# Kernel optimization log

Measured on AMD Instinct MI355X. Metric: run time of the kernel, lower is better.

The kernel has to match this reference:

```python
import jax, jax.numpy as jnp
import numpy as np

LEN_M = 131328   # (data_dim+1) * d_h = 513 * 256
D_H = 256
N_MC = 64
DATA_DIM_P1 = 513
N = 4096


def setup_inputs() -> dict:
    key = jax.random.key(0)
    k1, k2, k3, k4 = jax.random.split(key, 4)
    params = jax.random.normal(k1, (2 * LEN_M,), dtype=jnp.float32)
    W1 = jax.random.normal(k2, (D_H + 1,), dtype=jnp.float32)
    x = jax.random.normal(k3, (N, DATA_DIM_P1), dtype=jnp.float32)
    eps = jax.random.normal(k4, (N_MC,), dtype=jnp.float32)
    return {"params": params, "W1": W1, "x": x, "eps": eps}


def reference(params, W1, x, eps):
    # split variational params into means and (relu'd) variances
    m_w0 = params[:LEN_M]                                  # [len_m]
    v_w0 = jax.nn.relu(params[LEN_M:]) + 1e-6              # [len_m]
    # reparameterized MC sampling; NOTE: torch code draws ONE scalar eps per
    # MC sample (randn(m_w0[0].shape) is scalar), shared across all weights.
    samps_w0 = m_w0[:, None] + eps[None, :] * jnp.sqrt(v_w0)[:, None]  # [len_m, M]
    W0 = samps_w0.reshape(DATA_DIM_P1, D_H, N_MC)          # [d+1, h, M]
    # fused batched GEMM replacing the d_h * num_MC_samps tiny matmuls
    x_w0 = jnp.einsum('nd,dhm->nhm', x, W0)                # [N, h, M]
    z = jax.nn.relu(x_w0)
    ones = jnp.ones((x.shape[0], 1, N_MC), dtype=x.dtype)
    z = jnp.concatenate([ones, z], axis=1)                 # [N, h+1, M]
    pred_samps = jnp.einsum('nhm,h->nm', z, W1)            # [N, M]
    return pred_samps, m_w0, v_w0
```

## Files before the change

### kernel.cpp

```cpp
#include <hip/hip_runtime.h>
#include <hip/hip_bf16.h>
#include <math.h>

#define LEN_M   131328
#define D_P1    513
#define NROW    4096
#define PRED_ELEMS (NROW * 64)

typedef __attribute__((ext_vector_type(8))) short short8;
typedef __attribute__((ext_vector_type(4))) float floatx4;
typedef __attribute__((ext_vector_type(2))) float v2f;

__device__ __forceinline__ void gl_lds16(const void* g, void* l)
{
    __builtin_amdgcn_global_load_lds(
        (const __attribute__((address_space(1))) unsigned int*)g,
        (__attribute__((address_space(3))) unsigned int*)l, 16, 0, 0);
}

__device__ __forceinline__ unsigned short bf16b(float f)
{
    __hip_bfloat16 h = __float2bfloat16(f);
    return *(unsigned short*)&h;
}

__global__ __launch_bounds__(256) void prep_kernel(
    const float* __restrict__ params, float* __restrict__ out,
    __hip_bfloat16* __restrict__ wcbt)
{
    __shared__ unsigned short T[64][65];
    const int bid = blockIdx.x;
    const int t   = threadIdx.x;

    if (bid < 513) {
        int i = bid * 256 + t;
        float m = params[i];
        float v = fmaxf(params[LEN_M + i], 0.0f) + 1e-6f;
        out[PRED_ELEMS + i]         = m;
        out[PRED_ELEMS + LEN_M + i] = v;
        return;
    }
    if (bid < 769) {
        int i = (bid - 513) * 1024 + t * 4;
        float4 z = {0.f, 0.f, 0.f, 0.f};
        *(float4*)(out + i) = z;
        return;
    }

    const int b2 = bid - 769;
    const int k0 = (b2 & 7) * 64;
    const int c0 = (b2 >> 3) * 64;
    const int hh = t & 63, kb = t >> 6;
    const bool spart = (c0 >= 256);
    const int hbase = c0 & 255;
    const float* src = params + (spart ? LEN_M : 0);

    #pragma unroll 4
    for (int p = 0; p < 16; ++p) {
        int kk = p * 4 + kb;
        float v = src[(k0 + kk) * 256 + hbase + hh];
        if (spart) v = sqrtf(fmaxf(v, 0.0f) + 1e-6f);
        T[kk][hh] = bf16b(v);
    }
    __syncthreads();

    const int cc = t >> 2, kq = t & 3;
    short8 lo, hi;
    #pragma unroll
    for (int j = 0; j < 8; ++j) lo[j] = (short)T[kq * 16 + j][cc];
    #pragma unroll
    for (int j = 0; j < 8; ++j) hi[j] = (short)T[kq * 16 + 8 + j][cc];

    const int cR = c0 + cc;
    const int g1 = (k0 >> 3) + 2 * kq;
    const int g2 = g1 + 1;
    const int d1 = (g1 >> 3) * 4096 + cR * 8 + ((g1 & 7) ^ (cR & 7));
    const int d2 = (g2 >> 3) * 4096 + cR * 8 + ((g2 & 7) ^ (cR & 7));
    short* wb = (short*)wcbt;
    *(short8*)(wb + d1 * 8) = lo;
    *(short8*)(wb + d2 * 8) = hi;
}

__global__ __launch_bounds__(512) void main_kernel(
    const __hip_bfloat16* __restrict__ wcbt, const float* __restrict__ params,
    const float* __restrict__ x, const float* __restrict__ W1,
    const float* __restrict__ eps, float* __restrict__ out)
{
    extern __shared__ char smem[];
    char*  Ap = smem + 32768;
    float* Cl = (float*)smem;

    const int t = threadIdx.x;
    const int w = t >> 6, lane = t & 63;
    const int lane15 = lane & 15, quad = lane >> 4;
    const int ax7 = lane15 & 7;
    const int q  = blockIdx.x & 3;
    const int bm = (blockIdx.x >> 2) * 32;

    const char* wbase = (const char*)wcbt;

    int bsrc_c0, bsrc_c1;
    {
        int j0 = t, j1 = 512 + t;
        int lc0 = j0 >> 3, g0 = j0 & 7;
        int lc1 = j1 >> 3, g1 = j1 & 7;
        int cg0 = q * 64 + (lc0 & 63) + ((lc0 >> 6) * 256);
        int cg1 = q * 64 + (lc1 & 63) + ((lc1 >> 6) * 256);
        bsrc_c0 = cg0 * 8 + g0;
        bsrc_c1 = cg1 * 8 + g1;
    }

    gl_lds16(wbase + bsrc_c0 * 16, smem + t * 16);
    gl_lds16(wbase + bsrc_c1 * 16, smem + (512 + t) * 16);

    {
        const int r = t >> 4, seg0 = t & 15;
        const float* xrow = x + (bm + r) * D_P1;
        #pragma unroll
        for (int ss = 0; ss < 2; ++ss) {
            const int seg = seg0 + ss * 16;
            #pragma unroll
            for (int c2 = 0; c2 < 2; ++c2) {
                int g  = seg * 2 + c2;
                int cs = (g & ~7) | ((g & 7) ^ (r & 7));
                short8 pk;
                #pragma unroll
                for (int j = 0; j < 8; ++j)
                    pk[j] = (short)bf16b(xrow[seg * 16 + c2 * 8 + j]);
                *(short8*)(Ap + r * 1024 + cs * 16) = pk;
            }
        }
    }

    const float e = eps[lane];
    const int rh = w & 1;
    const int ct = w >> 1;
    float xl[4];
    #pragma unroll
    for (int i = 0; i < 4; ++i)
        xl[i] = x[(bm + rh * 16 + quad * 4 + i) * D_P1 + 512];
    const int gc0 = q * 64 + ct * 16 + lane15;
    const float wl0 = params[131072 + gc0];
    const float wl1 = sqrtf(fmaxf(params[LEN_M + 131072 + gc0], 0.0f) + 1e-6f);

    const int cb0 = (ct * 16 + lane15) * 128;
    const int cb1 = cb0 + 64 * 128;
    const char* Abase = Ap + (rh * 16 + lane15) * 1024;

    floatx4 acc0 = {0.f,0.f,0.f,0.f}, acc1 = acc0;

    __syncthreads();

    for (int kc = 0; kc < 8; ++kc) {
        if (kc < 7) {
            char* nbuf = smem + ((kc + 1) & 1) * 16384;
            const char* src = wbase + (kc + 1) * 65536;
            gl_lds16(src + bsrc_c0 * 16, nbuf + t * 16);
            gl_lds16(src + bsrc_c1 * 16, nbuf + (512 + t) * 16);
        }
        const char* Bb = smem + (kc & 1) * 16384;
        const char* Ab = Abase + kc * 128;
        #pragma unroll
        for (int kk = 0; kk < 2; ++kk) {
            const int off = ((kk * 4 + quad) ^ ax7) * 16;
            short8 a  = *(const short8*)(Ab + off);
            short8 b0 = *(const short8*)(Bb + cb0 + off);
            short8 b1 = *(const short8*)(Bb + cb1 + off);
            acc0 = __builtin_amdgcn_mfma_f32_16x16x32_bf16(a, b0, acc0, 0, 0, 0);
            acc1 = __builtin_amdgcn_mfma_f32_16x16x32_bf16(a, b1, acc1, 0, 0, 0);
        }
        __syncthreads();
    }

    {
        const int r0 = rh * 16 + quad * 4;
        float4 o0, o1;
        o0.x = acc0[0] + xl[0] * wl0;  o1.x = acc1[0] + xl[0] * wl1;
        o0.y = acc0[1] + xl[1] * wl0;  o1.y = acc1[1] + xl[1] * wl1;
        o0.z = acc0[2] + xl[2] * wl0;  o1.z = acc1[2] + xl[2] * wl1;
        o0.w = acc0[3] + xl[3] * wl0;  o1.w = acc1[3] + xl[3] * wl1;
        *(float4*)&Cl[(ct * 16 + lane15) * 36 + r0]      = o0;
        *(float4*)&Cl[(64 + ct * 16 + lane15) * 36 + r0] = o1;
    }
    __syncthreads();

    const int rw = w * 4;
    v2f accp0 = {0.f, 0.f}, accp1 = {0.f, 0.f};
    const v2f e2 = {e, e}, z2 = {0.f, 0.f};

    #pragma unroll 8
    for (int hh = 0; hh < 64; ++hh) {
        const float w1h = W1[1 + q * 64 + hh];
        const v2f w2 = {w1h, w1h};
        const float4 av = *(const float4*)&Cl[hh * 36 + rw];
        const float4 bv = *(const float4*)&Cl[(64 + hh) * 36 + rw];
        v2f a01 = {av.x, av.y}, a23 = {av.z, av.w};
        v2f b01 = {bv.x, bv.y}, b23 = {bv.z, bv.w};
        v2f t01 = __builtin_elementwise_max(__builtin_elementwise_fma(e2, b01, a01), z2);
        v2f t23 = __builtin_elementwise_max(__builtin_elementwise_fma(e2, b23, a23), z2);
        accp0 = __builtin_elementwise_fma(t01, w2, accp0);
        accp1 = __builtin_elementwise_fma(t23, w2, accp1);
    }
    if (q == 0) {
        const float b0 = W1[0];
        accp0.x += b0; accp0.y += b0; accp1.x += b0; accp1.y += b0;
    }

    float* op = out + (bm + rw) * 64 + lane;
    unsafeAtomicAdd(op,       accp0.x);
    unsafeAtomicAdd(op + 64,  accp0.y);
    unsafeAtomicAdd(op + 128, accp1.x);
    unsafeAtomicAdd(op + 192, accp1.y);
}

extern "C" void kernel_launch(void* const* d_in, const int* in_sizes, int n_in,
                              void* d_out, int out_size, void* d_ws, size_t ws_size,
                              hipStream_t stream)
{
    const float* params = (const float*)d_in[0];
    const float* W1     = (const float*)d_in[1];
    const float* x      = (const float*)d_in[2];
    const float* eps    = (const float*)d_in[3];
    float* out = (float*)d_out;
    __hip_bfloat16* wcbt = (__hip_bfloat16*)d_ws;

    static bool attr_set = false;
    if (!attr_set) {
        hipFuncSetAttribute((const void*)main_kernel,
                            hipFuncAttributeMaxDynamicSharedMemorySize, 65536);
        attr_set = true;
    }

    prep_kernel<<<833, 256, 0, stream>>>(params, out, wcbt);
    main_kernel<<<512, 512, 65536, stream>>>(wcbt, params, x, W1, eps, out);
}
```

Baseline: 82.11 us.

## Double the main kernel's row tile to 64 rows per block

Each main-kernel block now covers 64 rows of x instead of 32, so the grid shrinks from 512 to 256 blocks. Each warp computes a 16-row by 32-column slab for both the mean and the std parts, issuing four MFMAs per k-step instead of two. Every staged weight tile is reused across twice as many rows, halving global reads of the packed bf16 weights, and the epilogue handles 8 rows per warp with an enlarged LDS stride. The trade-off is 96 KB of LDS per block and half as many blocks, which may cut occupancy and latency hiding on a GPU with 256 compute units.

```diff
diff --git a/kernel.cpp b/kernel.cpp
--- a/kernel.cpp
+++ b/kernel.cpp
@@ -95,7 +95,7 @@
     const int lane15 = lane & 15, quad = lane >> 4;
     const int ax7 = lane15 & 7;
     const int q  = blockIdx.x & 3;
-    const int bm = (blockIdx.x >> 2) * 32;
+    const int bm = (blockIdx.x >> 2) * 64;
 
     const char* wbase = (const char*)wcbt;
 
@@ -114,11 +114,11 @@
     gl_lds16(wbase + bsrc_c1 * 16, smem + (512 + t) * 16);
 
     {
-        const int r = t >> 4, seg0 = t & 15;
+        const int r = t >> 3, seg0 = t & 7;
         const float* xrow = x + (bm + r) * D_P1;
         #pragma unroll
-        for (int ss = 0; ss < 2; ++ss) {
-            const int seg = seg0 + ss * 16;
+        for (int ss = 0; ss < 4; ++ss) {
+            const int seg = seg0 + ss * 8;
             #pragma unroll
             for (int c2 = 0; c2 < 2; ++c2) {
                 int g  = seg * 2 + c2;
@@ -133,21 +133,30 @@
     }
 
     const float e = eps[lane];
-    const int rh = w & 1;
-    const int ct = w >> 1;
+    const int rh = w & 3;
+    const int cw = w >> 2;
     float xl[4];
     #pragma unroll
     for (int i = 0; i < 4; ++i)
         xl[i] = x[(bm + rh * 16 + quad * 4 + i) * D_P1 + 512];
-    const int gc0 = q * 64 + ct * 16 + lane15;
-    const float wl0 = params[131072 + gc0];
-    const float wl1 = sqrtf(fmaxf(params[LEN_M + 131072 + gc0], 0.0f) + 1e-6f);
-
-    const int cb0 = (ct * 16 + lane15) * 128;
-    const int cb1 = cb0 + 64 * 128;
+    float wlm[2], wls[2];
+    #pragma unroll
+    for (int s = 0; s < 2; ++s) {
+        int gc = q * 64 + cw * 32 + s * 16 + lane15;
+        wlm[s] = params[131072 + gc];
+        wls[s] = sqrtf(fmaxf(params[LEN_M + 131072 + gc], 0.0f) + 1e-6f);
+    }
+
+    int cbm[2], cbs[2];
+    #pragma unroll
+    for (int s = 0; s < 2; ++s) {
+        int lc = cw * 32 + s * 16 + lane15;
+        cbm[s] = lc * 128;
+        cbs[s] = (lc + 64) * 128;
+    }
     const char* Abase = Ap + (rh * 16 + lane15) * 1024;
 
-    floatx4 acc0 = {0.f,0.f,0.f,0.f}, acc1 = acc0;
+    floatx4 am0 = {0.f,0.f,0.f,0.f}, am1 = am0, as0 = am0, as1 = am0;
 
     __syncthreads();
 
@@ -164,46 +173,64 @@
         for (int kk = 0; kk < 2; ++kk) {
             const int off = ((kk * 4 + quad) ^ ax7) * 16;
             short8 a  = *(const short8*)(Ab + off);
-            short8 b0 = *(const short8*)(Bb + cb0 + off);
-            short8 b1 = *(const short8*)(Bb + cb1 + off);
-            acc0 = __builtin_amdgcn_mfma_f32_16x16x32_bf16(a, b0, acc0, 0, 0, 0);
-            acc1 = __builtin_amdgcn_mfma_f32_16x16x32_bf16(a, b1, acc1, 0, 0, 0);
+            short8 b0 = *(const short8*)(Bb + cbm[0] + off);
+            short8 b1 = *(const short8*)(Bb + cbm[1] + off);
+            short8 b2 = *(const short8*)(Bb + cbs[0] + off);
+            short8 b3 = *(const short8*)(Bb + cbs[1] + off);
+            am0 = __builtin_amdgcn_mfma_f32_16x16x32_bf16(a, b0, am0, 0, 0, 0);
+            am1 = __builtin_amdgcn_mfma_f32_16x16x32_bf16(a, b1, am1, 0, 0, 0);
+            as0 = __builtin_amdgcn_mfma_f32_16x16x32_bf16(a, b2, as0, 0, 0, 0);
+            as1 = __builtin_amdgcn_mfma_f32_16x16x32_bf16(a, b3, as1, 0, 0, 0);
         }
         __syncthreads();
     }
 
     {
         const int r0 = rh * 16 + quad * 4;
-        float4 o0, o1;
-        o0.x = acc0[0] + xl[0] * wl0;  o1.x = acc1[0] + xl[0] * wl1;
-        o0.y = acc0[1] + xl[1] * wl0;  o1.y = acc1[1] + xl[1] * wl1;
-        o0.z = acc0[2] + xl[2] * wl0;  o1.z = acc1[2] + xl[2] * wl1;
-        o0.w = acc0[3] + xl[3] * wl0;  o1.w = acc1[3] + xl[3] * wl1;
-        *(float4*)&Cl[(ct * 16 + lane15) * 36 + r0]      = o0;
-        *(float4*)&Cl[(64 + ct * 16 + lane15) * 36 + r0] = o1;
+        floatx4 accm[2] = {am0, am1}, accs[2] = {as0, as1};
+        #pragma unroll
+        for (int s = 0; s < 2; ++s) {
+            float4 om, os;
+            om.x = accm[s][0] + xl[0] * wlm[s];  os.x = accs[s][0] + xl[0] * wls[s];
+            om.y = accm[s][1] + xl[1] * wlm[s];  os.y = accs[s][1] + xl[1] * wls[s];
+            om.z = accm[s][2] + xl[2] * wlm[s];  os.z = accs[s][2] + xl[2] * wls[s];
+            om.w = accm[s][3] + xl[3] * wlm[s];  os.w = accs[s][3] + xl[3] * wls[s];
+            const int lc = cw * 32 + s * 16 + lane15;
+            *(float4*)&Cl[lc * 68 + r0]        = om;
+            *(float4*)&Cl[(64 + lc) * 68 + r0] = os;
+        }
     }
     __syncthreads();
 
-    const int rw = w * 4;
-    v2f accp0 = {0.f, 0.f}, accp1 = {0.f, 0.f};
+    const int rw = w * 8;
+    v2f accp0 = {0.f,0.f}, accp1 = accp0, accp2 = accp0, accp3 = accp0;
     const v2f e2 = {e, e}, z2 = {0.f, 0.f};
 
     #pragma unroll 8
     for (int hh = 0; hh < 64; ++hh) {
         const float w1h = W1[1 + q * 64 + hh];
         const v2f w2 = {w1h, w1h};
-        const float4 av = *(const float4*)&Cl[hh * 36 + rw];
-        const float4 bv = *(const float4*)&Cl[(64 + hh) * 36 + rw];
-        v2f a01 = {av.x, av.y}, a23 = {av.z, av.w};
-        v2f b01 = {bv.x, bv.y}, b23 = {bv.z, bv.w};
-        v2f t01 = __builtin_elementwise_max(__builtin_elementwise_fma(e2, b01, a01), z2);
-        v2f t23 = __builtin_elementwise_max(__builtin_elementwise_fma(e2, b23, a23), z2);
-        accp0 = __builtin_elementwise_fma(t01, w2, accp0);
-        accp1 = __builtin_elementwise_fma(t23, w2, accp1);
+        const float4 av0 = *(const float4*)&Cl[hh * 68 + rw];
+        const float4 av1 = *(const float4*)&Cl[hh * 68 + rw + 4];
+        const float4 bv0 = *(const float4*)&Cl[(64 + hh) * 68 + rw];
+        const float4 bv1 = *(const float4*)&Cl[(64 + hh) * 68 + rw + 4];
+        v2f t0 = __builtin_elementwise_max(
+                     __builtin_elementwise_fma(e2, (v2f){bv0.x, bv0.y}, (v2f){av0.x, av0.y}), z2);
+        v2f t1 = __builtin_elementwise_max(
+                     __builtin_elementwise_fma(e2, (v2f){bv0.z, bv0.w}, (v2f){av0.z, av0.w}), z2);
+        v2f t2 = __builtin_elementwise_max(
+                     __builtin_elementwise_fma(e2, (v2f){bv1.x, bv1.y}, (v2f){av1.x, av1.y}), z2);
+        v2f t3 = __builtin_elementwise_max(
+                     __builtin_elementwise_fma(e2, (v2f){bv1.z, bv1.w}, (v2f){av1.z, av1.w}), z2);
+        accp0 = __builtin_elementwise_fma(t0, w2, accp0);
+        accp1 = __builtin_elementwise_fma(t1, w2, accp1);
+        accp2 = __builtin_elementwise_fma(t2, w2, accp2);
+        accp3 = __builtin_elementwise_fma(t3, w2, accp3);
     }
     if (q == 0) {
         const float b0 = W1[0];
         accp0.x += b0; accp0.y += b0; accp1.x += b0; accp1.y += b0;
+        accp2.x += b0; accp2.y += b0; accp3.x += b0; accp3.y += b0;
     }
 
     float* op = out + (bm + rw) * 64 + lane;
@@ -211,6 +238,10 @@
     unsafeAtomicAdd(op + 64,  accp0.y);
     unsafeAtomicAdd(op + 128, accp1.x);
     unsafeAtomicAdd(op + 192, accp1.y);
+    unsafeAtomicAdd(op + 256, accp2.x);
+    unsafeAtomicAdd(op + 320, accp2.y);
+    unsafeAtomicAdd(op + 384, accp3.x);
+    unsafeAtomicAdd(op + 448, accp3.y);
 }
 
 extern "C" void kernel_launch(void* const* d_in, const int* in_sizes, int n_in,
@@ -227,10 +258,10 @@
     static bool attr_set = false;
     if (!attr_set) {
         hipFuncSetAttribute((const void*)main_kernel,
-                            hipFuncAttributeMaxDynamicSharedMemorySize, 65536);
+                            hipFuncAttributeMaxDynamicSharedMemorySize, 98304);
         attr_set = true;
     }
 
     prep_kernel<<<833, 256, 0, stream>>>(params, out, wcbt);
-    main_kernel<<<512, 512, 65536, stream>>>(wcbt, params, x, W1, eps, out);
-}
+    main_kernel<<<256, 512, 98304, stream>>>(wcbt, params, x, W1, eps, out);
+}
```

New measurement: 84.49 us. 1.03x slower.
